# Kernel tuning notes

Hardware: AMD Instinct MI355X
Metric: run time of the kernel (lower is better)

## Reference

```python
import jax, jax.numpy as jnp
import numpy as np

B, W = 256, 512
FEAT, TIME, OV_IN, OV = 128, 32, 32, 32
IN = FEAT + TIME + OV  # 192
HG, HL = 256, 128
OG, OL = 128, 64


def _p(key, shape, scale):
    return (jax.random.normal(key, shape, dtype=jnp.float32) * scale)


def setup_inputs() -> dict:
    key = jax.random.key(0)
    ks = jax.random.split(key, 24)
    d = {
        'f_seq': jax.random.normal(ks[0], (B, W, FEAT), dtype=jnp.float32),
        'delta_seq': jax.random.normal(ks[1], (B, W, TIME), dtype=jnp.float32),
        'overlap_seq': jax.random.normal(ks[2], (B, W, OV_IN), dtype=jnp.float32),
        # overlap encoder: Linear(32,64) -> SiLU -> Linear(64,32)
        'W1': _p(ks[3], (64, OV_IN), 1.0 / np.sqrt(OV_IN)),
        'b1': _p(ks[4], (64,), 0.02),
        'W2': _p(ks[5], (OV, 64), 1.0 / np.sqrt(64)),
        'b2': _p(ks[6], (OV,), 0.02),
        # global GRUCell (PyTorch layout: [r; z; n] stacked)
        'Wih_g': _p(ks[7], (3 * HG, IN), 1.0 / np.sqrt(HG)),
        'Whh_g': _p(ks[8], (3 * HG, HG), 1.0 / np.sqrt(HG)),
        'bih_g': _p(ks[9], (3 * HG,), 0.02),
        'bhh_g': _p(ks[10], (3 * HG,), 0.02),
        # local GRUCell
        'Wih_l': _p(ks[11], (3 * HL, IN), 1.0 / np.sqrt(HL)),
        'Whh_l': _p(ks[12], (3 * HL, HL), 1.0 / np.sqrt(HL)),
        'bih_l': _p(ks[13], (3 * HL,), 0.02),
        'bhh_l': _p(ks[14], (3 * HL,), 0.02),
        # output projections
        'Wg': _p(ks[15], (OG, HG), 1.0 / np.sqrt(HG)),
        'bg': _p(ks[16], (OG,), 0.02),
        'Wl': _p(ks[17], (OL, HL), 1.0 / np.sqrt(HL)),
        'bl': _p(ks[18], (OL,), 0.02),
    }
    return d


def _gru_scan(x_ih_seq, h0, Whh, bhh):
    # x_ih_seq: (W, B, 3H) precomputed input gates; returns hidden states (W, B, H)
    def step(h, xih):
        gh = h @ Whh.T + bhh
        xr, xz, xn = jnp.split(xih, 3, axis=-1)
        hr, hz, hn = jnp.split(gh, 3, axis=-1)
        r = jax.nn.sigmoid(xr + hr)
        z = jax.nn.sigmoid(xz + hz)
        n = jnp.tanh(xn + r * hn)
        h_new = (1.0 - z) * n + z * h
        return h_new, h_new
    _, hs = jax.lax.scan(step, h0, x_ih_seq)
    return hs


def _forward(f_seq, delta_seq, overlap_seq, W1, b1, W2, b2,
             Wih_g, Whh_g, bih_g, bhh_g, Wih_l, Whh_l, bih_l, bhh_l,
             Wg, bg, Wl, bl):
    # overlap encoder applied to whole sequence (time-independent)
    ov = jax.nn.silu(overlap_seq @ W1.T + b1) @ W2.T + b2  # (B, W, OV)
    inp = jnp.concatenate([f_seq, delta_seq, ov], axis=-1)  # (B, W, IN)
    # precompute input-to-hidden gates for all timesteps (batched GEMM)
    xih_g = (inp @ Wih_g.T + bih_g).transpose(1, 0, 2)  # (W, B, 3HG)
    xih_l = (inp @ Wih_l.T + bih_l).transpose(1, 0, 2)  # (W, B, 3HL)
    h_g0 = jnp.zeros((inp.shape[0], Whh_g.shape[1]), dtype=inp.dtype)
    h_l0 = jnp.zeros((inp.shape[0], Whh_l.shape[1]), dtype=inp.dtype)
    hg_seq = _gru_scan(xih_g, h_g0, Whh_g, bhh_g)  # (W, B, HG)
    hl_seq = _gru_scan(xih_l, h_l0, Whh_l, bhh_l)  # (W, B, HL)
    g_seq = (hg_seq @ Wg.T + bg).transpose(1, 0, 2)  # (B, W, OG)
    m_seq = (hl_seq @ Wl.T + bl).transpose(1, 0, 2)  # (B, W, OL)
    return g_seq, m_seq


def reference(f_seq, delta_seq, overlap_seq, W1, b1, W2, b2,
              Wih_g, Whh_g, bih_g, bhh_g, Wih_l, Whh_l, bih_l, bhh_l,
              Wg, bg, Wl, bl):
    return _forward(f_seq, delta_seq, overlap_seq, W1, b1, W2, b2,
                    Wih_g, Whh_g, bih_g, bhh_g, Wih_l, Whh_l, bih_l, bhh_l,
                    Wg, bg, Wl, bl)
```

## Files before the change

### kernel.cpp

```cpp
#include <hip/hip_runtime.h>

typedef _Float16 f16;
typedef _Float16 f16x2 __attribute__((ext_vector_type(2)));
typedef _Float16 f16x8 __attribute__((ext_vector_type(8)));
typedef float f32x4 __attribute__((ext_vector_type(4)));
typedef unsigned int u32;

static constexpr size_t NROWS = 131072;
static constexpr int TC = 64;
static constexpr int NCHUNK = 8;
static constexpr size_t CROWS = 256 * TC;

static constexpr size_t O_INP = 0;
static constexpr size_t SZ_INP = NROWS * 192 * 2;
static constexpr size_t O_XB  = O_INP + SZ_INP;
static constexpr size_t SZ_XB = CROWS * 1152 * 2;
static constexpr size_t O_HG  = O_XB + SZ_XB;
static constexpr size_t SZ_HG = NROWS * 256 * 2;
static constexpr size_t O_HL  = O_HG + SZ_HG;
static constexpr size_t SZ_HL = NROWS * 128 * 2;
static constexpr size_t O_WF  = O_HL + SZ_HL;
static constexpr size_t SZ_WF = 1152 * 192 * 2;
static constexpr size_t O_BF  = O_WF + SZ_WF;
static constexpr size_t SZ_BF = 1152 * 4;
static constexpr size_t O_WHG = O_BF + SZ_BF;
static constexpr size_t SZ_WHG = 128 * 768 * 4;
static constexpr size_t O_WHL = O_WHG + SZ_WHG;
static constexpr size_t SZ_WHL = 64 * 384 * 4;
static constexpr size_t O_WG  = O_WHL + SZ_WHL;
static constexpr size_t SZ_WG = 128 * 256 * 2;
static constexpr size_t O_WL  = O_WG + SZ_WG;
static constexpr size_t SZ_WL = 64 * 128 * 2;
static constexpr size_t O_HGF = O_WL + SZ_WL;
static constexpr size_t SZ_HGF = 256 * 256 * 4;
static constexpr size_t O_HGP = O_HGF + SZ_HGF;
static constexpr size_t SZ_HGP = 256 * 128 * 4;
static constexpr size_t O_HLF = O_HGP + SZ_HGP;
static constexpr size_t SZ_HLF = 256 * 128 * 4;
static constexpr size_t O_HLP = O_HLF + SZ_HLF;
static constexpr size_t SZ_HLP = 256 * 64 * 4;
static constexpr size_t WS_NEED = O_HLP + SZ_HLP;

__device__ inline u32 pk2f(float lo, float hi) {
  f16x2 t; t.x = (f16)lo; t.y = (f16)hi;
  return __builtin_bit_cast(u32, t);
}

#if defined(__has_builtin)
#if __has_builtin(__builtin_amdgcn_fdot2)
#define HAVE_FDOT2 1
#endif
#endif

__device__ inline float dot2f(u32 w, u32 h, float c) {
#ifdef HAVE_FDOT2
  return __builtin_amdgcn_fdot2(__builtin_bit_cast(f16x2, w),
                                __builtin_bit_cast(f16x2, h), c, false);
#else
  f16x2 a = __builtin_bit_cast(f16x2, w);
  f16x2 b = __builtin_bit_cast(f16x2, h);
  return c + (float)a.x * (float)b.x + (float)a.y * (float)b.y;
#endif
}

__device__ inline float sigf(float x) { return 1.f / (1.f + __expf(-x)); }
__device__ inline float tanhf_fast(float x) { return 1.f - 2.f / (1.f + __expf(2.f * x)); }

__global__ void prep_k(const float* __restrict__ Wih_g, const float* __restrict__ Wih_l,
                       const float* __restrict__ bih_g, const float* __restrict__ bih_l,
                       const float* __restrict__ Whh_g, const float* __restrict__ Whh_l,
                       const float* __restrict__ Wg, const float* __restrict__ Wl,
                       f16* __restrict__ wfused, float* __restrict__ biasf,
                       u32* __restrict__ whhg, u32* __restrict__ whhl,
                       f16* __restrict__ wg16, f16* __restrict__ wl16) {
  const int tid = blockIdx.x * blockDim.x + threadIdx.x;
  const int stride = gridDim.x * blockDim.x;
  for (int i = tid; i < 1152 * 192; i += stride) {
    int r = i / 192;
    wfused[i] = (f16)(r < 768 ? Wih_g[i] : Wih_l[i - 768 * 192]);
  }
  for (int i = tid; i < 1152; i += stride)
    biasf[i] = (i < 768) ? bih_g[i] : bih_l[i - 768];
  for (int i = tid; i < 128 * 768; i += stride) {
    int k2 = i / 768, r = i % 768;
    whhg[i] = pk2f(Whh_g[r * 256 + 2 * k2], Whh_g[r * 256 + 2 * k2 + 1]);
  }
  for (int i = tid; i < 64 * 384; i += stride) {
    int k2 = i / 384, r = i % 384;
    whhl[i] = pk2f(Whh_l[r * 128 + 2 * k2], Whh_l[r * 128 + 2 * k2 + 1]);
  }
  for (int i = tid; i < 128 * 256; i += stride) wg16[i] = (f16)Wg[i];
  for (int i = tid; i < 64 * 128; i += stride) wl16[i] = (f16)Wl[i];
}

__global__ __launch_bounds__(256) void encoder_k(
    const float* __restrict__ f_seq, const float* __restrict__ delta,
    const float* __restrict__ ovin, const float* __restrict__ W1,
    const float* __restrict__ b1, const float* __restrict__ W2,
    const float* __restrict__ b2, f16* __restrict__ inp) {
  __shared__ float sW1[2048], sW2[2048], sb1[64], sb2[32];
  for (int i = threadIdx.x; i < 2048; i += 256) { sW1[i] = W1[i]; sW2[i] = W2[i]; }
  if (threadIdx.x < 64) sb1[threadIdx.x] = b1[threadIdx.x];
  if (threadIdx.x < 32) sb2[threadIdx.x] = b2[threadIdx.x];
  __syncthreads();
  const size_t rid = (size_t)blockIdx.x * 256 + threadIdx.x;
  const size_t b = rid >> 9, t = rid & 511;

  float ov[32];
  const float4* ovp = reinterpret_cast<const float4*>(ovin + rid * 32);
#pragma unroll
  for (int i = 0; i < 8; ++i) {
    float4 v = ovp[i];
    ov[4 * i] = v.x; ov[4 * i + 1] = v.y; ov[4 * i + 2] = v.z; ov[4 * i + 3] = v.w;
  }
  float hb[64];
#pragma unroll
  for (int j = 0; j < 64; ++j) {
    float s = sb1[j];
#pragma unroll
    for (int k = 0; k < 32; ++k) s += sW1[j * 32 + k] * ov[k];
    hb[j] = s * sigf(s);
  }
  u32* orow = reinterpret_cast<u32*>(inp + (t * 256 + b) * 192);
  const float4* fp = reinterpret_cast<const float4*>(f_seq + rid * 128);
#pragma unroll
  for (int i = 0; i < 32; ++i) {
    float4 v = fp[i];
    orow[2 * i] = pk2f(v.x, v.y); orow[2 * i + 1] = pk2f(v.z, v.w);
  }
  const float4* dp = reinterpret_cast<const float4*>(delta + rid * 32);
#pragma unroll
  for (int i = 0; i < 8; ++i) {
    float4 v = dp[i];
    orow[64 + 2 * i] = pk2f(v.x, v.y); orow[64 + 2 * i + 1] = pk2f(v.z, v.w);
  }
#pragma unroll
  for (int p = 0; p < 16; ++p) {
    float s0 = sb2[2 * p], s1 = sb2[2 * p + 1];
#pragma unroll
    for (int j = 0; j < 64; ++j) {
      s0 += sW2[(2 * p) * 64 + j] * hb[j];
      s1 += sW2[(2 * p + 1) * 64 + j] * hb[j];
    }
    orow[80 + p] = pk2f(s0, s1);
  }
}

template <int K, int NROWSB, int NVALID, bool OUTF16, int LDC>
__global__ __launch_bounds__(256, 2) void gemm_f16k(
    const f16* __restrict__ A, const f16* __restrict__ Bw,
    const float* __restrict__ bias, void* __restrict__ Cout) {
  __shared__ alignas(16) f16 At[128 * 40];
  __shared__ alignas(16) f16 Bt[128 * 40];
  const int n0 = blockIdx.x * 128;
  const int m0 = blockIdx.y * 128;
  const int tid = threadIdx.x;
  const int l = tid & 63;
  const int w = tid >> 6;
  const int wm = w >> 1, wn = w & 1;
  const int srow = tid >> 2, schunk = tid & 3;

  f32x4 acc[4][4] = {};

  for (int k0 = 0; k0 < K; k0 += 32) {
#pragma unroll
    for (int hh = 0; hh < 2; ++hh) {
      int row = srow + hh * 64;
      uint4 av = *reinterpret_cast<const uint4*>(A + (size_t)(m0 + row) * K + k0 + schunk * 8);
      *reinterpret_cast<uint4*>(&At[row * 40 + schunk * 8]) = av;
      int nr = n0 + row;
      uint4 bv = make_uint4(0u, 0u, 0u, 0u);
      if (nr < NROWSB)
        bv = *reinterpret_cast<const uint4*>(Bw + (size_t)nr * K + k0 + schunk * 8);
      *reinterpret_cast<uint4*>(&Bt[row * 40 + schunk * 8]) = bv;
    }
    __syncthreads();
    f16x8 af[4], bf[4];
#pragma unroll
    for (int i = 0; i < 4; ++i) {
      af[i] = *reinterpret_cast<const f16x8*>(&At[(wm * 64 + i * 16 + (l & 15)) * 40 + (l >> 4) * 8]);
      bf[i] = *reinterpret_cast<const f16x8*>(&Bt[(wn * 64 + i * 16 + (l & 15)) * 40 + (l >> 4) * 8]);
    }
#pragma unroll
    for (int mi = 0; mi < 4; ++mi)
#pragma unroll
      for (int ni = 0; ni < 4; ++ni)
        acc[mi][ni] = __builtin_amdgcn_mfma_f32_16x16x32_f16(af[mi], bf[ni], acc[mi][ni], 0, 0, 0);
    __syncthreads();
  }

  const int mbase = m0 + wm * 64 + ((l >> 4) << 2);
  const int nbase = n0 + wn * 64 + (l & 15);
#pragma unroll
  for (int mi = 0; mi < 4; ++mi) {
#pragma unroll
    for (int ni = 0; ni < 4; ++ni) {
      int n = nbase + ni * 16;
      if (n < NVALID) {
        float bsv = bias[n];
#pragma unroll
        for (int q = 0; q < 4; ++q) {
          int m = mbase + mi * 16 + q;
          float v = acc[mi][ni][q] + bsv;
          if constexpr (OUTF16)
            reinterpret_cast<f16*>(Cout)[(size_t)m * LDC + n] = (f16)v;
          else
            reinterpret_cast<float*>(Cout)[(size_t)m * LDC + n] = v;
        }
      }
    }
  }
}

__global__ __launch_bounds__(768, 3) void gru_global_k(
    const u32* __restrict__ whh, const float* __restrict__ bhh,
    const f16* __restrict__ xbuf, u32* __restrict__ hseq,
    float* __restrict__ hstf, u32* __restrict__ hstp, int t0) {
  __shared__ alignas(16) u32 hpk[128];
  __shared__ float hfs[256];
  __shared__ float rz[512];
  const int b = blockIdx.x;
  const int r = threadIdx.x;

  u32 wv[128];
#pragma unroll
  for (int i = 0; i < 128; ++i) wv[i] = whh[i * 768 + r];
  const float bh = bhh[r];

  if (t0 == 0) {
    if (r < 256) hfs[r] = 0.f;
    if (r < 128) hpk[r] = 0u;
  } else {
    if (r < 256) hfs[r] = hstf[b * 256 + r];
    if (r < 128) hpk[r] = hstp[b * 128 + r];
  }
  __syncthreads();

  const f16* xp = xbuf + (size_t)b * 1152 + r;
  u32* hout = hseq + (size_t)b * 512 * 128 + (size_t)t0 * 128;
  float xv = (float)xp[0];

  for (int t = 0; t < TC; ++t) {
    float xnext = 0.f;
    if (t < TC - 1) xnext = (float)xp[(size_t)(t + 1) * 256 * 1152];

    float a0 = 0.f, a1 = 0.f, a2 = 0.f, a3 = 0.f;
#pragma unroll
    for (int q = 0; q < 32; ++q) {
      uint4 hq = reinterpret_cast<const uint4*>(hpk)[q];
      a0 = dot2f(wv[4 * q + 0], hq.x, a0);
      a1 = dot2f(wv[4 * q + 1], hq.y, a1);
      a2 = dot2f(wv[4 * q + 2], hq.z, a2);
      a3 = dot2f(wv[4 * q + 3], hq.w, a3);
    }
    float gh = ((a0 + a1) + (a2 + a3)) + bh;

    if (r < 512) rz[r] = sigf(xv + gh);
    __syncthreads();
    if (r >= 512) {
      int j = r - 512;
      float rv = rz[j];
      float zv = rz[256 + j];
      float nv = tanhf_fast(xv + rv * gh);
      float hold = hfs[j];
      float hnew = (1.f - zv) * nv + zv * hold;
      hfs[j] = hnew;
      float hpart = __shfl_xor(hnew, 1, 64);
      if ((j & 1) == 0) {
        u32 packed = pk2f(hnew, hpart);
        hpk[j >> 1] = packed;
        hout[(size_t)t * 128 + (j >> 1)] = packed;
      }
    }
    __syncthreads();
    xv = xnext;
  }
  if (r < 256) hstf[b * 256 + r] = hfs[r];
  if (r < 128) hstp[b * 128 + r] = hpk[r];
}

__global__ __launch_bounds__(384, 2) void gru_local_k(
    const u32* __restrict__ whh, const float* __restrict__ bhh,
    const f16* __restrict__ xbuf, u32* __restrict__ hseq,
    float* __restrict__ hstf, u32* __restrict__ hstp, int t0) {
  __shared__ alignas(16) u32 hpk[64];
  __shared__ float hfs[128];
  __shared__ float rz[256];
  const int b = blockIdx.x;
  const int r = threadIdx.x;

  u32 wv[64];
#pragma unroll
  for (int i = 0; i < 64; ++i) wv[i] = whh[i * 384 + r];
  const float bh = bhh[r];

  if (t0 == 0) {
    if (r < 128) hfs[r] = 0.f;
    if (r < 64) hpk[r] = 0u;
  } else {
    if (r < 128) hfs[r] = hstf[b * 128 + r];
    if (r < 64) hpk[r] = hstp[b * 64 + r];
  }
  __syncthreads();

  const f16* xp = xbuf + (size_t)b * 1152 + 768 + r;
  u32* hout = hseq + (size_t)b * 512 * 64 + (size_t)t0 * 64;
  float xv = (float)xp[0];

  for (int t = 0; t < TC; ++t) {
    float xnext = 0.f;
    if (t < TC - 1) xnext = (float)xp[(size_t)(t + 1) * 256 * 1152];

    float a0 = 0.f, a1 = 0.f, a2 = 0.f, a3 = 0.f;
#pragma unroll
    for (int q = 0; q < 16; ++q) {
      uint4 hq = reinterpret_cast<const uint4*>(hpk)[q];
      a0 = dot2f(wv[4 * q + 0], hq.x, a0);
      a1 = dot2f(wv[4 * q + 1], hq.y, a1);
      a2 = dot2f(wv[4 * q + 2], hq.z, a2);
      a3 = dot2f(wv[4 * q + 3], hq.w, a3);
    }
    float gh = ((a0 + a1) + (a2 + a3)) + bh;

    if (r < 256) rz[r] = sigf(xv + gh);
    __syncthreads();
    if (r >= 256) {
      int j = r - 256;
      float rv = rz[j];
      float zv = rz[128 + j];
      float nv = tanhf_fast(xv + rv * gh);
      float hold = hfs[j];
      float hnew = (1.f - zv) * nv + zv * hold;
      hfs[j] = hnew;
      float hpart = __shfl_xor(hnew, 1, 64);
      if ((j & 1) == 0) {
        u32 packed = pk2f(hnew, hpart);
        hpk[j >> 1] = packed;
        hout[(size_t)t * 64 + (j >> 1)] = packed;
      }
    }
    __syncthreads();
    xv = xnext;
  }
  if (r < 128) hstf[b * 128 + r] = hfs[r];
  if (r < 64) hstp[b * 64 + r] = hpk[r];
}

extern "C" void kernel_launch(void* const* d_in, const int* in_sizes, int n_in,
                              void* d_out, int out_size, void* d_ws, size_t ws_size,
                              hipStream_t stream) {
  (void)in_sizes; (void)n_in; (void)out_size;
  if (ws_size < WS_NEED) return;
  const float* f_seq = (const float*)d_in[0];
  const float* delta = (const float*)d_in[1];
  const float* ovseq = (const float*)d_in[2];
  const float* W1 = (const float*)d_in[3];
  const float* b1 = (const float*)d_in[4];
  const float* W2 = (const float*)d_in[5];
  const float* b2 = (const float*)d_in[6];
  const float* Wih_g = (const float*)d_in[7];
  const float* Whh_g = (const float*)d_in[8];
  const float* bih_g = (const float*)d_in[9];
  const float* bhh_g = (const float*)d_in[10];
  const float* Wih_l = (const float*)d_in[11];
  const float* Whh_l = (const float*)d_in[12];
  const float* bih_l = (const float*)d_in[13];
  const float* bhh_l = (const float*)d_in[14];
  const float* Wg = (const float*)d_in[15];
  const float* bg = (const float*)d_in[16];
  const float* Wl = (const float*)d_in[17];
  const float* bl = (const float*)d_in[18];

  char* ws = (char*)d_ws;
  f16* inp = (f16*)(ws + O_INP);
  f16* xbuf = (f16*)(ws + O_XB);
  f16* hg16 = (f16*)(ws + O_HG);
  f16* hl16 = (f16*)(ws + O_HL);
  f16* wfused = (f16*)(ws + O_WF);
  float* biasf = (float*)(ws + O_BF);
  u32* whhg = (u32*)(ws + O_WHG);
  u32* whhl = (u32*)(ws + O_WHL);
  f16* wg16 = (f16*)(ws + O_WG);
  f16* wl16 = (f16*)(ws + O_WL);
  float* hgf = (float*)(ws + O_HGF);
  u32* hgp = (u32*)(ws + O_HGP);
  float* hlf = (float*)(ws + O_HLF);
  u32* hlp = (u32*)(ws + O_HLP);

  float* outg = (float*)d_out;
  float* outm = outg + NROWS * 128;

  prep_k<<<dim3(256), dim3(256), 0, stream>>>(Wih_g, Wih_l, bih_g, bih_l, Whh_g, Whh_l,
                                              Wg, Wl, wfused, biasf, whhg, whhl, wg16, wl16);
  encoder_k<<<dim3(512), dim3(256), 0, stream>>>(f_seq, delta, ovseq, W1, b1, W2, b2, inp);

  for (int c = 0; c < NCHUNK; ++c) {
    const f16* Ac = inp + (size_t)c * CROWS * 192;
    gemm_f16k<192, 1152, 1152, true, 1152><<<dim3(9, CROWS / 128), dim3(256), 0, stream>>>(
        Ac, wfused, biasf, xbuf);
    gru_global_k<<<dim3(256), dim3(768), 0, stream>>>(whhg, bhh_g, xbuf, (u32*)hg16, hgf, hgp, c * TC);
    gru_local_k<<<dim3(256), dim3(384), 0, stream>>>(whhl, bhh_l, xbuf, (u32*)hl16, hlf, hlp, c * TC);
  }

  gemm_f16k<256, 128, 128, false, 128><<<dim3(1, 1024), dim3(256), 0, stream>>>(hg16, wg16, bg, outg);
  gemm_f16k<128, 64, 64, false, 64><<<dim3(1, 1024), dim3(256), 0, stream>>>(hl16, wl16, bl, outm);
}
```

Measured before the change: 1.732 ms.

## Split encoder into coalesced copy kernels and remap time-major rows inside input GEMM

Replaces the monolithic encoder, which wrote a transposed time-major inp with one thread per row (uncoalesced), with separate coalesced copy kernels for f_seq and delta plus an overlap-encoder kernel, all writing inp in batch-major order. The transpose moves into the input-projection GEMM, which now remaps each A-row index to batch-major addressing using the chunk's time base. This should make encoder memory traffic coalesced, at the cost of three launches instead of one and strided A-row gathers in the GEMM.

```diff
diff --git a/kernel.cpp b/kernel.cpp
--- a/kernel.cpp
+++ b/kernel.cpp
@@ -93,8 +93,25 @@
   for (int i = tid; i < 64 * 128; i += stride) wl16[i] = (f16)Wl[i];
 }
 
-__global__ __launch_bounds__(256) void encoder_k(
-    const float* __restrict__ f_seq, const float* __restrict__ delta,
+__global__ __launch_bounds__(256) void copy_f_k(const float* __restrict__ f_seq,
+                                                f16* __restrict__ inp) {
+  const size_t idx = (size_t)blockIdx.x * 256 + threadIdx.x;
+  const float4 v = reinterpret_cast<const float4*>(f_seq)[idx];
+  const size_t row = idx >> 5, c4 = idx & 31;
+  uint2 pr; pr.x = pk2f(v.x, v.y); pr.y = pk2f(v.z, v.w);
+  *reinterpret_cast<uint2*>(reinterpret_cast<u32*>(inp) + row * 96 + 2 * c4) = pr;
+}
+
+__global__ __launch_bounds__(256) void copy_d_k(const float* __restrict__ delta,
+                                                f16* __restrict__ inp) {
+  const size_t idx = (size_t)blockIdx.x * 256 + threadIdx.x;
+  const float4 v = reinterpret_cast<const float4*>(delta)[idx];
+  const size_t row = idx >> 3, c4 = idx & 7;
+  uint2 pr; pr.x = pk2f(v.x, v.y); pr.y = pk2f(v.z, v.w);
+  *reinterpret_cast<uint2*>(reinterpret_cast<u32*>(inp) + row * 96 + 64 + 2 * c4) = pr;
+}
+
+__global__ __launch_bounds__(256) void ovenc_k(
     const float* __restrict__ ovin, const float* __restrict__ W1,
     const float* __restrict__ b1, const float* __restrict__ W2,
     const float* __restrict__ b2, f16* __restrict__ inp) {
@@ -103,11 +120,10 @@
   if (threadIdx.x < 64) sb1[threadIdx.x] = b1[threadIdx.x];
   if (threadIdx.x < 32) sb2[threadIdx.x] = b2[threadIdx.x];
   __syncthreads();
-  const size_t rid = (size_t)blockIdx.x * 256 + threadIdx.x;
-  const size_t b = rid >> 9, t = rid & 511;
+  const size_t row = (size_t)blockIdx.x * 256 + threadIdx.x;
 
   float ov[32];
-  const float4* ovp = reinterpret_cast<const float4*>(ovin + rid * 32);
+  const float4* ovp = reinterpret_cast<const float4*>(ovin + row * 32);
 #pragma unroll
   for (int i = 0; i < 8; ++i) {
     float4 v = ovp[i];
@@ -121,19 +137,7 @@
     for (int k = 0; k < 32; ++k) s += sW1[j * 32 + k] * ov[k];
     hb[j] = s * sigf(s);
   }
-  u32* orow = reinterpret_cast<u32*>(inp + (t * 256 + b) * 192);
-  const float4* fp = reinterpret_cast<const float4*>(f_seq + rid * 128);
-#pragma unroll
-  for (int i = 0; i < 32; ++i) {
-    float4 v = fp[i];
-    orow[2 * i] = pk2f(v.x, v.y); orow[2 * i + 1] = pk2f(v.z, v.w);
-  }
-  const float4* dp = reinterpret_cast<const float4*>(delta + rid * 32);
-#pragma unroll
-  for (int i = 0; i < 8; ++i) {
-    float4 v = dp[i];
-    orow[64 + 2 * i] = pk2f(v.x, v.y); orow[64 + 2 * i + 1] = pk2f(v.z, v.w);
-  }
+  u32* orow = reinterpret_cast<u32*>(inp) + row * 96 + 80;
 #pragma unroll
   for (int p = 0; p < 16; ++p) {
     float s0 = sb2[2 * p], s1 = sb2[2 * p + 1];
@@ -142,14 +146,14 @@
       s0 += sW2[(2 * p) * 64 + j] * hb[j];
       s1 += sW2[(2 * p + 1) * 64 + j] * hb[j];
     }
-    orow[80 + p] = pk2f(s0, s1);
-  }
-}
-
-template <int K, int NROWSB, int NVALID, bool OUTF16, int LDC>
+    orow[p] = pk2f(s0, s1);
+  }
+}
+
+template <int K, int NROWSB, int NVALID, bool OUTF16, int LDC, bool REMAP>
 __global__ __launch_bounds__(256, 2) void gemm_f16k(
     const f16* __restrict__ A, const f16* __restrict__ Bw,
-    const float* __restrict__ bias, void* __restrict__ Cout) {
+    const float* __restrict__ bias, void* __restrict__ Cout, int t_base) {
   __shared__ alignas(16) f16 At[128 * 40];
   __shared__ alignas(16) f16 Bt[128 * 40];
   const int n0 = blockIdx.x * 128;
@@ -166,7 +170,10 @@
 #pragma unroll
     for (int hh = 0; hh < 2; ++hh) {
       int row = srow + hh * 64;
-      uint4 av = *reinterpret_cast<const uint4*>(A + (size_t)(m0 + row) * K + k0 + schunk * 8);
+      int m = m0 + row;
+      size_t g = REMAP ? ((size_t)(m & 255) * 512 + (size_t)t_base + (size_t)(m >> 8))
+                       : (size_t)m;
+      uint4 av = *reinterpret_cast<const uint4*>(A + g * K + k0 + schunk * 8);
       *reinterpret_cast<uint4*>(&At[row * 40 + schunk * 8]) = av;
       int nr = n0 + row;
       uint4 bv = make_uint4(0u, 0u, 0u, 0u);
@@ -392,16 +399,17 @@
 
   prep_k<<<dim3(256), dim3(256), 0, stream>>>(Wih_g, Wih_l, bih_g, bih_l, Whh_g, Whh_l,
                                               Wg, Wl, wfused, biasf, whhg, whhl, wg16, wl16);
-  encoder_k<<<dim3(512), dim3(256), 0, stream>>>(f_seq, delta, ovseq, W1, b1, W2, b2, inp);
+  copy_f_k<<<dim3(NROWS * 32 / 256), dim3(256), 0, stream>>>(f_seq, inp);
+  copy_d_k<<<dim3(NROWS * 8 / 256), dim3(256), 0, stream>>>(delta, inp);
+  ovenc_k<<<dim3(512), dim3(256), 0, stream>>>(ovseq, W1, b1, W2, b2, inp);
 
   for (int c = 0; c < NCHUNK; ++c) {
-    const f16* Ac = inp + (size_t)c * CROWS * 192;
-    gemm_f16k<192, 1152, 1152, true, 1152><<<dim3(9, CROWS / 128), dim3(256), 0, stream>>>(
-        Ac, wfused, biasf, xbuf);
+    gemm_f16k<192, 1152, 1152, true, 1152, true><<<dim3(9, CROWS / 128), dim3(256), 0, stream>>>(
+        inp, wfused, biasf, xbuf, c * TC);
     gru_global_k<<<dim3(256), dim3(768), 0, stream>>>(whhg, bhh_g, xbuf, (u32*)hg16, hgf, hgp, c * TC);
     gru_local_k<<<dim3(256), dim3(384), 0, stream>>>(whhl, bhh_l, xbuf, (u32*)hl16, hlf, hlp, c * TC);
   }
 
-  gemm_f16k<256, 128, 128, false, 128><<<dim3(1, 1024), dim3(256), 0, stream>>>(hg16, wg16, bg, outg);
-  gemm_f16k<128, 64, 64, false, 64><<<dim3(1, 1024), dim3(256), 0, stream>>>(hl16, wl16, bl, outm);
-}
+  gemm_f16k<256, 128, 128, false, 128, false><<<dim3(1, 1024), dim3(256), 0, stream>>>(hg16, wg16, bg, outg, 0);
+  gemm_f16k<128, 64, 64, false, 64, false><<<dim3(1, 1024), dim3(256), 0, stream>>>(hl16, wl16, bl, outm, 0);
+}
```

Result: faster. 1.612 ms (-6.9%).
